# Kernel optimization log

Measured on AMD Instinct MI355X. Metric: run time of the kernel, lower is better.

The kernel has to match this reference:

```python
import jax, jax.numpy as jnp
import numpy as np

NUM_HEADS = 16
HIDDEN = 1024
HEAD_DIM = HIDDEN // NUM_HEADS


def setup_inputs() -> dict:
    key = jax.random.key(0)
    ks = jax.random.split(key, 9)
    B, S = 2, 2048
    s = 1.0 / np.sqrt(HIDDEN)
    return {
        "x": jax.random.normal(ks[0], (B, S, HIDDEN), dtype=jnp.float32),
        "Wq": jax.random.normal(ks[1], (HIDDEN, HIDDEN), dtype=jnp.float32) * s,
        "bq": jnp.zeros((HIDDEN,), dtype=jnp.float32),
        "Wk": jax.random.normal(ks[2], (HIDDEN, HIDDEN), dtype=jnp.float32) * s,
        "bk": jnp.zeros((HIDDEN,), dtype=jnp.float32),
        "Wv": jax.random.normal(ks[3], (HIDDEN, HIDDEN), dtype=jnp.float32) * s,
        "bv": jnp.zeros((HIDDEN,), dtype=jnp.float32),
        "Wo": jax.random.normal(ks[4], (HIDDEN, HIDDEN), dtype=jnp.float32) * s,
        "bo": jnp.zeros((HIDDEN,), dtype=jnp.float32),
    }


def reference(x, Wq, bq, Wk, bk, Wv, bv, Wo, bo):
    B, S, H = x.shape
    # project and split heads: [B, S, H] -> [B, nh, S, hd]
    def split_heads(t):
        return t.reshape(B, S, NUM_HEADS, HEAD_DIM).transpose(0, 2, 1, 3)

    q = split_heads(x @ Wq + bq)
    k = split_heads(x @ Wk + bk)
    v = split_heads(x @ Wv + bv)

    scores = jnp.einsum("bhqd,bhkd->bhqk", q, k) / jnp.sqrt(
        jnp.asarray(HEAD_DIM, dtype=x.dtype))
    probs = jax.nn.softmax(scores, axis=-1)
    # attn_drop_rate = 0.0 -> dropout is identity
    ctx = jnp.einsum("bhqk,bhkd->bhqd", probs, v)
    ctx = ctx.transpose(0, 2, 1, 3).reshape(B, S, H)
    out = ctx @ Wo + bo
    return out
```

## Files before the change

### kernel.cpp

```cpp
#include <hip/hip_runtime.h>

#define NHEADS 16
#define HDIM   64
#define SEQL   2048
#define HID    1024
#define NB     2
#define MT     4096

#define QSCALE 0.18033688011112042f

typedef float        f4_t   __attribute__((ext_vector_type(4)));
typedef float        f32x16 __attribute__((ext_vector_type(16)));
typedef unsigned int u32x4  __attribute__((ext_vector_type(4)));
typedef __bf16       bf16x8 __attribute__((ext_vector_type(8)));

typedef const __attribute__((address_space(1))) unsigned int* gas_ptr;
typedef __attribute__((address_space(3))) unsigned int*       las_ptr;

__device__ __forceinline__ void gload16(const void* g, void* l){
  __builtin_amdgcn_global_load_lds((gas_ptr)g, (las_ptr)l, 16, 0, 0);
}
__device__ __forceinline__ unsigned int pkbf(float a, float b){
  unsigned short lo = __builtin_bit_cast(unsigned short, (__bf16)a);
  unsigned short hi = __builtin_bit_cast(unsigned short, (__bf16)b);
  return (unsigned)lo | ((unsigned)hi << 16);
}
__device__ __forceinline__ unsigned short f2bf(float f){
  return __builtin_bit_cast(unsigned short, (__bf16)f);
}
__device__ __forceinline__ float bf2f(unsigned short h){
  return __uint_as_float(((unsigned int)h) << 16);
}
__device__ __forceinline__ u32x4 ld16(const unsigned short* p){
  return *reinterpret_cast<const u32x4*>(p);
}
__device__ __forceinline__ f4_t mfma_bf16(u32x4 a, u32x4 b, f4_t c){
  return __builtin_amdgcn_mfma_f32_16x16x32_bf16(
      __builtin_bit_cast(bf16x8, a), __builtin_bit_cast(bf16x8, b), c, 0, 0, 0);
}
__device__ __forceinline__ f32x16 mfma32(u32x4 a, u32x4 b, f32x16 c){
  return __builtin_amdgcn_mfma_f32_32x32x16_bf16(
      __builtin_bit_cast(bf16x8, a), __builtin_bit_cast(bf16x8, b), c, 0, 0, 0);
}

#if __has_builtin(__builtin_amdgcn_permlane32_swap)
typedef unsigned int u32x2 __attribute__((ext_vector_type(2)));
__device__ __forceinline__ void plswap(unsigned int &a, unsigned int &b){
  u32x2 r = __builtin_amdgcn_permlane32_swap(a, b, false, false);
  a = r[0]; b = r[1];
}
#else
__device__ __forceinline__ void plswap(unsigned int &a, unsigned int &b){
  unsigned int as = (unsigned int)__shfl_xor((int)a, 32);
  unsigned int bs = (unsigned int)__shfl_xor((int)b, 32);
  bool hi = (threadIdx.x & 32) != 0;
  unsigned int na = hi ? bs : a;
  unsigned int nb = hi ? b  : as;
  a = na; b = nb;
}
#endif

__global__ __launch_bounds__(256) void prep(
    const float* __restrict__ x,
    const float* __restrict__ Wq, const float* __restrict__ Wk,
    const float* __restrict__ Wv, const float* __restrict__ Wo,
    unsigned short* __restrict__ xb,
    unsigned short* __restrict__ wqT, unsigned short* __restrict__ wkT,
    unsigned short* __restrict__ wvT, unsigned short* __restrict__ woT){
  __shared__ float t[32][33];
  const int id = blockIdx.x;
  if (id < 4096) {
    int z = id >> 10;
    int rem = id & 1023;
    const float* W = (z==0)?Wq:(z==1)?Wk:(z==2)?Wv:Wo;
    unsigned short* WT = (z==0)?wqT:(z==1)?wkT:(z==2)?wvT:woT;
    float sc = (z==0) ? QSCALE : 1.0f;
    int k0 = (rem >> 5)*32, n0 = (rem & 31)*32;
    int tx = threadIdx.x & 31, ty = threadIdx.x >> 5;
    #pragma unroll
    for (int ii=0; ii<4; ii++)
      t[ty+ii*8][tx] = W[(k0+ty+ii*8)*HID + n0+tx];
    __syncthreads();
    #pragma unroll
    for (int ii=0; ii<4; ii++)
      WT[(n0+ty+ii*8)*HID + k0+tx] = f2bf(t[tx][ty+ii*8] * sc);
  } else {
    int gid = (id - 4096)*256 + threadIdx.x;
    float4 a = reinterpret_cast<const float4*>(x)[gid * 2];
    float4 b = reinterpret_cast<const float4*>(x)[gid * 2 + 1];
    u32x4 o;
    o[0] = pkbf(a.x, a.y);
    o[1] = pkbf(a.z, a.w);
    o[2] = pkbf(b.x, b.y);
    o[3] = pkbf(b.z, b.w);
    *reinterpret_cast<u32x4*>(&xb[gid * 8]) = o;
  }
}

__global__ __launch_bounds__(256) void qkv_gemm(
    const unsigned short* __restrict__ xb,
    const unsigned short* __restrict__ wqT, const unsigned short* __restrict__ wkT,
    const unsigned short* __restrict__ wvT,
    const float* __restrict__ bq, const float* __restrict__ bk, const float* __restrict__ bv,
    unsigned short* __restrict__ qo, unsigned short* __restrict__ ko,
    unsigned short* __restrict__ vto){
  __shared__ unsigned short As[2][128*32];
  __shared__ unsigned short Bs[2][128*32];
  const int z = blockIdx.z;
  const unsigned short* wT = (z==0)?wqT:(z==1)?wkT:wvT;
  const float* bias = (z==0)?bq:(z==1)?bk:bv;
  const float bscale = (z==0) ? QSCALE : 1.0f;
  const int m0 = blockIdx.x * 128;
  const int n0 = blockIdx.y * 128;
  const int tid = threadIdx.x;
  const int lane = tid & 63, w = tid >> 6;
  const int l15 = lane & 15, lg = lane >> 4;
  const int wr = (w >> 1) * 64, wc = (w & 1) * 64;
  const int srow = w*16 + (lane >> 2);
  const int skc  = (lane & 3) * 8;

  f4_t acc[4][4];
  f4_t z4 = {0.f, 0.f, 0.f, 0.f};
  #pragma unroll
  for (int i=0;i<4;i++)
    #pragma unroll
    for (int j=0;j<4;j++) acc[i][j] = z4;

  auto stageg = [&](int buf, int kt){
    #pragma unroll
    for (int c = 0; c < 2; c++) {
      int row = c*64 + srow;
      gload16(&xb[(m0+row)*HID + kt + skc], (char*)As[buf] + c*4096 + w*1024);
      gload16(&wT[(n0+row)*HID + kt + skc], (char*)Bs[buf] + c*4096 + w*1024);
    }
  };

  stageg(0, 0);
  int cur = 0;
  for (int kt = 0; kt < HID; kt += 32) {
    __syncthreads();
    if (kt + 32 < HID) stageg(cur^1, kt + 32);
    u32x4 a[4], b[4];
    #pragma unroll
    for (int i=0;i<4;i++) a[i] = ld16(&As[cur][(wr + i*16 + l15)*32 + lg*8]);
    #pragma unroll
    for (int j=0;j<4;j++) b[j] = ld16(&Bs[cur][(wc + j*16 + l15)*32 + lg*8]);
    __builtin_amdgcn_s_setprio(1);
    #pragma unroll
    for (int i=0;i<4;i++)
      #pragma unroll
      for (int j=0;j<4;j++)
        acc[i][j] = mfma_bf16(a[i], b[j], acc[i][j]);
    __builtin_amdgcn_s_setprio(0);
    cur ^= 1;
  }
  if (z == 2) {
    #pragma unroll
    for (int i=0;i<4;i++){
      int mrow = m0 + wr + i*16 + lg*4;
      int b_ = mrow >> 11, s = mrow & 2047;
      #pragma unroll
      for (int j=0;j<4;j++){
        int n = n0 + wc + j*16 + l15;
        float bs = bias[n];
        int h = n >> 6, d = n & 63;
        unsigned int lo = pkbf(acc[i][j][0]+bs, acc[i][j][1]+bs);
        unsigned int hi = pkbf(acc[i][j][2]+bs, acc[i][j][3]+bs);
        unsigned long long v8 = (unsigned long long)lo | ((unsigned long long)hi << 32);
        *reinterpret_cast<unsigned long long*>(
            vto + (((b_*NHEADS + h)*HDIM + d)*SEQL + s)) = v8;
      }
    }
  } else {
    unsigned short* outp = (z==0) ? qo : ko;
    #pragma unroll
    for (int i=0;i<4;i++){
      int mrow = m0 + wr + i*16 + lg*4;
      #pragma unroll
      for (int j=0;j<4;j++){
        int n = n0 + wc + j*16 + l15;
        float bs = bias[n] * bscale;
        int h = n >> 6, d = n & 63;
        #pragma unroll
        for (int r=0;r<4;r++){
          int m = mrow + r;
          int b_ = m >> 11, s = m & 2047;
          outp[(((b_*NHEADS + h)*SEQL) + s)*HDIM + d] = f2bf(acc[i][j][r] + bs);
        }
      }
    }
  }
}

__global__ __launch_bounds__(256, 4) void flash(
    const unsigned short* __restrict__ q,
    const unsigned short* __restrict__ k,
    const unsigned short* __restrict__ vT,
    unsigned short* __restrict__ po,
    float* __restrict__ pl,
    int kspan){
  __shared__ unsigned short Ks[2][4096];
  __shared__ unsigned short Vs[2][4096];
  const int bh = blockIdx.y;
  const int z = blockIdx.z;
  const int kb0 = z * kspan;
  const int tid = threadIdx.x;
  const int w = tid >> 6, lane = tid & 63;
  const int l31 = lane & 31, hi = lane >> 5;
  const int q0 = blockIdx.x*128 + w*32;
  const unsigned short* qb = q + (bh*SEQL + q0)*HDIM;
  const unsigned short* kp = k + bh*SEQL*HDIM;
  const unsigned short* vp = vT + bh*HDIM*SEQL;

  const int sr = w*16 + (lane >> 3);
  const int scol = ((lane & 7) ^ (sr & 7)) * 8;
  const int ldst = w*2048;

  u32x4 qf[4];
  #pragma unroll
  for (int c=0;c<4;c++)
    qf[c] = ld16(&qb[l31*HDIM + c*16 + hi*8]);

  u32x4 ones;
  ones[0] = 0x3F803F80u; ones[1] = 0x3F803F80u;
  ones[2] = 0x3F803F80u; ones[3] = 0x3F803F80u;

  f32x16 oacc[2], lsacc;
  f32x16 z16 = {0.f,0.f,0.f,0.f,0.f,0.f,0.f,0.f,0.f,0.f,0.f,0.f,0.f,0.f,0.f,0.f};
  oacc[0] = z16; oacc[1] = z16; lsacc = z16;

  auto stage = [&](int buf, int kb){
    const unsigned short* gk = kp + (kb + sr)*HDIM + scol;
    gload16(gk,          (char*)Ks[buf] + ldst);
    gload16(gk + 8*HDIM, (char*)Ks[buf] + ldst + 1024);
    const unsigned short* gv = vp + sr*SEQL + kb + scol;
    gload16(gv,          (char*)Vs[buf] + ldst);
    gload16(gv + 8*SEQL, (char*)Vs[buf] + ldst + 1024);
  };

  int cur = 0;
  stage(0, kb0);
  __syncthreads();

  const int rs = (l31 & 7) << 4;

  for (int kb = kb0; kb < kb0 + kspan; kb += 64) {
    if (kb + 64 < kb0 + kspan) stage(cur^1, kb + 64);
    const char* kbase = (const char*)Ks[cur];
    const char* vbase = (const char*)Vs[cur];

    f32x16 sacc[2];
    __builtin_amdgcn_s_setprio(1);
    #pragma unroll
    for (int t=0;t<2;t++){
      const char* rowb = kbase + (t*32 + l31)*128;
      #pragma unroll
      for (int c=0;c<4;c++){
        u32x4 kf = *reinterpret_cast<const u32x4*>(rowb + ((c*32 + hi*16) ^ rs));
        sacc[t] = (c==0) ? mfma32(kf, qf[0], z16) : mfma32(kf, qf[c], sacc[t]);
      }
    }
    __builtin_amdgcn_s_setprio(0);

    #pragma unroll
    for (int t=0;t<2;t++)
      #pragma unroll
      for (int r=0;r<16;r++) sacc[t][r] = exp2f(sacc[t][r]);

    u32x4 pa[4];
    #pragma unroll
    for (int t=0;t<2;t++)
      #pragma unroll
      for (int hf=0;hf<2;hf++){
        unsigned int c1 = pkbf(sacc[t][hf*8+0], sacc[t][hf*8+1]);
        unsigned int c2 = pkbf(sacc[t][hf*8+2], sacc[t][hf*8+3]);
        unsigned int c3 = pkbf(sacc[t][hf*8+4], sacc[t][hf*8+5]);
        unsigned int c4 = pkbf(sacc[t][hf*8+6], sacc[t][hf*8+7]);
        plswap(c1, c3);
        plswap(c2, c4);
        u32x4 f; f[0]=c1; f[1]=c2; f[2]=c3; f[3]=c4;
        pa[t*2+hf] = f;
      }

    __builtin_amdgcn_s_setprio(1);
    #pragma unroll
    for (int dt=0;dt<2;dt++){
      const char* rowb = vbase + (dt*32 + l31)*128;
      #pragma unroll
      for (int ks=0;ks<4;ks++){
        u32x4 vf = *reinterpret_cast<const u32x4*>(rowb + ((ks*32 + hi*16) ^ rs));
        oacc[dt] = mfma32(vf, pa[ks], oacc[dt]);
      }
    }
    #pragma unroll
    for (int ks=0;ks<4;ks++)
      lsacc = mfma32(ones, pa[ks], lsacc);
    __builtin_amdgcn_s_setprio(0);
    __syncthreads();
    cur ^= 1;
  }

  const int rowi = (z*NB*NHEADS + bh)*SEQL + q0 + l31;
  unsigned short* pb = po + (size_t)rowi*HDIM;
  #pragma unroll
  for (int dt=0;dt<2;dt++){
    #pragma unroll
    for (int kq=0;kq<4;kq++){
      unsigned int lo = pkbf(oacc[dt][kq*4+0], oacc[dt][kq*4+1]);
      unsigned int hv = pkbf(oacc[dt][kq*4+2], oacc[dt][kq*4+3]);
      unsigned long long v8 = (unsigned long long)lo | ((unsigned long long)hv << 32);
      *reinterpret_cast<unsigned long long*>(pb + dt*32 + kq*8 + hi*4) = v8;
    }
  }
  if (hi == 0) pl[rowi] = lsacc[0];
}

__global__ __launch_bounds__(256) void combine(
    const unsigned short* __restrict__ po, const float* __restrict__ pl,
    unsigned short* __restrict__ ctx, int nsplit){
  int i = blockIdx.x*256 + threadIdx.x;
  int dq = i & 15;
  int rsi = i >> 4;
  int bh = rsi >> 11, s = rsi & 2047;
  int b_ = bh >> 4, h = bh & 15;
  float L = pl[rsi];
  ushort4 o0 = reinterpret_cast<const ushort4*>(po)[rsi*16 + dq];
  float ax = bf2f(o0.x), ay = bf2f(o0.y), az = bf2f(o0.z), aw = bf2f(o0.w);
  if (nsplit == 2) {
    ushort4 o1 = reinterpret_cast<const ushort4*>(po)[rsi*16 + dq + NB*NHEADS*SEQL*16];
    L += pl[rsi + NB*NHEADS*SEQL];
    ax += bf2f(o1.x); ay += bf2f(o1.y); az += bf2f(o1.z); aw += bf2f(o1.w);
  }
  float inv = 1.0f / L;
  unsigned int lo = pkbf(ax*inv, ay*inv);
  unsigned int hv = pkbf(az*inv, aw*inv);
  unsigned long long v8 = (unsigned long long)lo | ((unsigned long long)hv << 32);
  *reinterpret_cast<unsigned long long*>(
      ctx + (b_*SEQL + s)*HID + h*HDIM + dq*4) = v8;
}

__global__ __launch_bounds__(256) void out_gemm(
    const unsigned short* __restrict__ cb,
    const unsigned short* __restrict__ woT,
    const float* __restrict__ bo,
    float* __restrict__ out){
  __shared__ unsigned short As[2][64*32];
  __shared__ unsigned short Bs[2][128*32];
  const int m0 = blockIdx.x * 64;
  const int n0 = blockIdx.y * 128;
  const int tid = threadIdx.x;
  const int lane = tid & 63, w = tid >> 6;
  const int l15 = lane & 15, lg = lane >> 4;
  const int wr = (w >> 1) * 32, wc = (w & 1) * 64;
  const int srow = w*16 + (lane >> 2);
  const int skc  = (lane & 3) * 8;

  f4_t acc[2][4];
  f4_t z4 = {0.f,0.f,0.f,0.f};
  #pragma unroll
  for (int i=0;i<2;i++)
    #pragma unroll
    for (int j=0;j<4;j++) acc[i][j] = z4;

  auto stageg = [&](int buf, int kt){
    gload16(&cb[(m0+srow)*HID + kt + skc], (char*)As[buf] + w*1024);
    #pragma unroll
    for (int c = 0; c < 2; c++) {
      int row = c*64 + srow;
      gload16(&woT[(n0+row)*HID + kt + skc], (char*)Bs[buf] + c*4096 + w*1024);
    }
  };

  stageg(0, 0);
  int cur = 0;
  for (int kt = 0; kt < HID; kt += 32) {
    __syncthreads();
    if (kt + 32 < HID) stageg(cur^1, kt + 32);
    u32x4 a[2], b[4];
    #pragma unroll
    for (int i=0;i<2;i++) a[i] = ld16(&As[cur][(wr + i*16 + l15)*32 + lg*8]);
    #pragma unroll
    for (int j=0;j<4;j++) b[j] = ld16(&Bs[cur][(wc + j*16 + l15)*32 + lg*8]);
    __builtin_amdgcn_s_setprio(1);
    #pragma unroll
    for (int i=0;i<2;i++)
      #pragma unroll
      for (int j=0;j<4;j++)
        acc[i][j] = mfma_bf16(a[i], b[j], acc[i][j]);
    __builtin_amdgcn_s_setprio(0);
    cur ^= 1;
  }
  #pragma unroll
  for (int i=0;i<2;i++){
    int mrow = m0 + wr + i*16 + lg*4;
    #pragma unroll
    for (int j=0;j<4;j++){
      int n = n0 + wc + j*16 + l15;
      float bs = bo[n];
      #pragma unroll
      for (int r=0;r<4;r++)
        out[(mrow + r)*HID + n] = acc[i][j][r] + bs;
    }
  }
}

extern "C" void kernel_launch(void* const* d_in, const int* in_sizes, int n_in,
                              void* d_out, int out_size, void* d_ws, size_t ws_size,
                              hipStream_t stream){
  const float* x  = (const float*)d_in[0];
  const float* Wq = (const float*)d_in[1];
  const float* bq = (const float*)d_in[2];
  const float* Wk = (const float*)d_in[3];
  const float* bk = (const float*)d_in[4];
  const float* Wv = (const float*)d_in[5];
  const float* bv = (const float*)d_in[6];
  const float* Wo = (const float*)d_in[7];
  const float* bo = (const float*)d_in[8];
  float* out = (float*)d_out;

  char* ws = (char*)d_ws;
  size_t off = 0;
  auto alloc = [&](size_t bytes) -> void* {
    void* p = ws + off;
    off += (bytes + 255) & ~(size_t)255;
    return p;
  };
  unsigned short* xb   = (unsigned short*)alloc((size_t)MT*HID*2);
  unsigned short* wqT  = (unsigned short*)alloc((size_t)HID*HID*2);
  unsigned short* wkT  = (unsigned short*)alloc((size_t)HID*HID*2);
  unsigned short* wvT  = (unsigned short*)alloc((size_t)HID*HID*2);
  unsigned short* woT  = (unsigned short*)alloc((size_t)HID*HID*2);
  unsigned short* q_ws = (unsigned short*)alloc((size_t)MT*HID*2);
  unsigned short* k_ws = (unsigned short*)alloc((size_t)MT*HID*2);
  unsigned short* vT_ws= (unsigned short*)alloc((size_t)MT*HID*2);
  unsigned short* c_ws = (unsigned short*)alloc((size_t)MT*HID*2);
  size_t base_off = off;

  int nsplit = 1;
  {
    size_t need2 = base_off + (((size_t)2*MT*HID*2 + 255) & ~(size_t)255)
                            + (((size_t)2*NB*NHEADS*SEQL*4 + 255) & ~(size_t)255);
    if (ws_size >= need2) nsplit = 2;
  }
  unsigned short* po = (unsigned short*)alloc((size_t)nsplit*MT*HID*2);
  float* pl = (float*)alloc((size_t)nsplit*NB*NHEADS*SEQL*4);
  int kspan = SEQL / nsplit;

  prep<<<dim3(6144), dim3(256), 0, stream>>>(x, Wq,Wk,Wv,Wo, xb,
                                             wqT,wkT,wvT,woT);
  qkv_gemm<<<dim3(32,8,3), dim3(256), 0, stream>>>(xb, wqT,wkT,wvT, bq,bk,bv,
                                                   q_ws, k_ws, vT_ws);
  flash<<<dim3(16,32,nsplit), dim3(256), 0, stream>>>(q_ws, k_ws, vT_ws,
                                                      po, pl, kspan);
  combine<<<dim3(MT*HID/4/256), dim3(256), 0, stream>>>(po, pl, c_ws, nsplit);
  out_gemm<<<dim3(64,8), dim3(256), 0, stream>>>(c_ws, woT, bo, out);
}
```

Measured before the change: 144.2 us.

## Stage 128-key tiles per barrier in flash attention loop

Doubles the K/V tile staged into LDS per iteration from 64 to 128 keys and processes it as two 64-key halves, with the V layout and swizzle reworked for 256-byte rows. This halves the number of __syncthreads and loop iterations per key span and issues more async loads per stage. In exchange LDS use doubles to 64KB per block and the occupancy hint in launch_bounds is dropped, which may reduce resident blocks per CU. It also assumes kspan is a multiple of 128.

New measurement: 151.9 us. 5.4% more time.

```diff
diff --git a/kernel.cpp b/kernel.cpp
--- a/kernel.cpp
+++ b/kernel.cpp
@@ -192,15 +192,15 @@
   }
 }
 
-__global__ __launch_bounds__(256, 4) void flash(
+__global__ __launch_bounds__(256) void flash(
     const unsigned short* __restrict__ q,
     const unsigned short* __restrict__ k,
     const unsigned short* __restrict__ vT,
     unsigned short* __restrict__ po,
     float* __restrict__ pl,
     int kspan){
-  __shared__ unsigned short Ks[2][4096];
-  __shared__ unsigned short Vs[2][4096];
+  __shared__ unsigned short Ks[2][8192];
+  __shared__ unsigned short Vs[2][8192];
   const int bh = blockIdx.y;
   const int z = blockIdx.z;
   const int kb0 = z * kspan;
@@ -212,9 +212,12 @@
   const unsigned short* kp = k + bh*SEQL*HDIM;
   const unsigned short* vp = vT + bh*HDIM*SEQL;
 
-  const int sr = w*16 + (lane >> 3);
-  const int scol = ((lane & 7) ^ (sr & 7)) * 8;
-  const int ldst = w*2048;
+  const int krow = w*32 + (lane >> 3);
+  const int kcol = ((lane & 7) ^ (krow & 7)) * 8;
+  const int vrow = w*16 + (lane >> 4);
+  const int vslot = lane & 15;
+  const int vcolA = (vslot ^ (vrow & 7)) * 8;
+  const int vcolB = (vslot ^ ((vrow + 4) & 7)) * 8;
 
   u32x4 qf[4];
   #pragma unroll
@@ -230,25 +233,21 @@
   oacc[0] = z16; oacc[1] = z16; lsacc = z16;
 
   auto stage = [&](int buf, int kb){
-    const unsigned short* gk = kp + (kb + sr)*HDIM + scol;
-    gload16(gk,          (char*)Ks[buf] + ldst);
-    gload16(gk + 8*HDIM, (char*)Ks[buf] + ldst + 1024);
-    const unsigned short* gv = vp + sr*SEQL + kb + scol;
-    gload16(gv,          (char*)Vs[buf] + ldst);
-    gload16(gv + 8*SEQL, (char*)Vs[buf] + ldst + 1024);
+    #pragma unroll
+    for (int j=0;j<4;j++)
+      gload16(kp + (kb + krow + j*8)*HDIM + kcol,
+              (char*)Ks[buf] + w*4096 + j*1024);
+    #pragma unroll
+    for (int j=0;j<4;j++){
+      int sc = (j & 1) ? vcolB : vcolA;
+      gload16(vp + (vrow + j*4)*SEQL + kb + sc,
+              (char*)Vs[buf] + w*4096 + j*1024);
+    }
   };
 
-  int cur = 0;
-  stage(0, kb0);
-  __syncthreads();
-
   const int rs = (l31 & 7) << 4;
 
-  for (int kb = kb0; kb < kb0 + kspan; kb += 64) {
-    if (kb + 64 < kb0 + kspan) stage(cur^1, kb + 64);
-    const char* kbase = (const char*)Ks[cur];
-    const char* vbase = (const char*)Vs[cur];
-
+  auto compute64 = [&](const char* kbase, const char* vbase, int hoff){
     f32x16 sacc[2];
     __builtin_amdgcn_s_setprio(1);
     #pragma unroll
@@ -261,12 +260,10 @@
       }
     }
     __builtin_amdgcn_s_setprio(0);
-
     #pragma unroll
     for (int t=0;t<2;t++)
       #pragma unroll
       for (int r=0;r<16;r++) sacc[t][r] = exp2f(sacc[t][r]);
-
     u32x4 pa[4];
     #pragma unroll
     for (int t=0;t<2;t++)
@@ -281,11 +278,10 @@
         u32x4 f; f[0]=c1; f[1]=c2; f[2]=c3; f[3]=c4;
         pa[t*2+hf] = f;
       }
-
     __builtin_amdgcn_s_setprio(1);
     #pragma unroll
     for (int dt=0;dt<2;dt++){
-      const char* rowb = vbase + (dt*32 + l31)*128;
+      const char* rowb = vbase + (dt*32 + l31)*256 + hoff;
       #pragma unroll
       for (int ks=0;ks<4;ks++){
         u32x4 vf = *reinterpret_cast<const u32x4*>(rowb + ((ks*32 + hi*16) ^ rs));
@@ -296,6 +292,16 @@
     for (int ks=0;ks<4;ks++)
       lsacc = mfma32(ones, pa[ks], lsacc);
     __builtin_amdgcn_s_setprio(0);
+  };
+
+  int cur = 0;
+  stage(0, kb0);
+  __syncthreads();
+
+  for (int kb = kb0; kb < kb0 + kspan; kb += 128) {
+    if (kb + 128 < kb0 + kspan) stage(cur^1, kb + 128);
+    compute64((const char*)Ks[cur],        (const char*)Vs[cur], 0);
+    compute64((const char*)Ks[cur] + 8192, (const char*)Vs[cur], 128);
     __syncthreads();
     cur ^= 1;
   }
```
